# Performance work log

Hardware: AMD Instinct MI355X
Metric: run time of the kernel (lower is better)

Reference implementation:

```python
import jax, jax.numpy as jnp
import numpy as np

D_MODEL = 768
N_HEAD = 12
D_K = D_MODEL // N_HEAD  # 64, also d_v
B, S = 2, 2048


def setup_inputs() -> dict:
    key = jax.random.key(0)
    ks = jax.random.split(key, 8)
    scale = 1.0 / np.sqrt(D_MODEL)
    return {
        "q": jax.random.normal(ks[0], (B, S, D_MODEL), dtype=jnp.float32),
        "k": jax.random.normal(ks[1], (B, S, D_MODEL), dtype=jnp.float32),
        "v": jax.random.normal(ks[2], (B, S, D_MODEL), dtype=jnp.float32),
        "mask": jax.random.randint(ks[3], (B, 1, S, S), 0, 2, dtype=jnp.int32),
        # per-head projection weights, stacked over heads: [H, d_model, d_k]
        "Wq": jax.random.normal(ks[4], (N_HEAD, D_MODEL, D_K), dtype=jnp.float32) * scale,
        "Wk": jax.random.normal(ks[5], (N_HEAD, D_MODEL, D_K), dtype=jnp.float32) * scale,
        "Wv": jax.random.normal(ks[6], (N_HEAD, D_MODEL, D_K), dtype=jnp.float32) * scale,
        # output projection: [n_head*d_v, d_model]
        "Wo": jax.random.normal(ks[7], (N_HEAD * D_K, D_MODEL), dtype=jnp.float32) * scale,
    }


def reference(q, k, v, mask, Wq, Wk, Wv, Wo):
    # Per-head projections (batched over heads instead of a python loop)
    qh = jnp.einsum("bsd,hdk->bhsk", q, Wq)  # [B,H,S,d_k]
    kh = jnp.einsum("bsd,hdk->bhsk", k, Wk)
    vh = jnp.einsum("bsd,hdk->bhsk", v, Wv)
    # Scaled dot-product attention with full score matrix (faithful to source)
    scores = jnp.einsum("bhsk,bhtk->bhst", qh, kh) / jnp.sqrt(jnp.asarray(D_K, qh.dtype))
    scores = jnp.where(mask == 0, jnp.asarray(-1e9, scores.dtype), scores)
    attn = jax.nn.softmax(scores, axis=-1)  # [B,H,S,S]
    out = jnp.einsum("bhst,bhtk->bhsk", attn, vh)  # [B,H,S,d_k]
    # concat heads (matches torch.cat over head outputs along last dim)
    out = out.transpose(0, 2, 1, 3).reshape(out.shape[0], out.shape[2], -1)  # [B,S,H*d_k]
    return out @ Wo  # [B,S,d_model]
```

## Files before the change

### kernel.cpp

```cpp
#include <hip/hip_runtime.h>
#include <stdint.h>

#define S_LEN 2048
#define NH 12
#define DM 768
#define DK 64
#define NB 2
#define MROWS (NB * S_LEN)

typedef __attribute__((ext_vector_type(8))) short short8;
typedef __attribute__((ext_vector_type(4))) float f32x4;
typedef __attribute__((ext_vector_type(4))) uint32_t u32x4;

__device__ __forceinline__ unsigned short bf16rne(float f) {
    union { float f; uint32_t u; } v; v.f = f;
    return (unsigned short)((v.u + 0x7FFFu + ((v.u >> 16) & 1u)) >> 16);
}

__device__ __forceinline__ uint32_t cvtpk(float lo, float hi) {
    uint32_t r;
    asm("v_cvt_pk_bf16_f32 %0, %1, %2" : "=v"(r) : "v"(lo), "v"(hi));
    return r;
}

__global__ __launch_bounds__(256) void prep_kernel(
        const float* __restrict__ Wq, const float* __restrict__ Wk,
        const float* __restrict__ Wv, const float* __restrict__ Wo,
        const int* __restrict__ mask,
        unsigned short* __restrict__ WqT, unsigned short* __restrict__ WkT,
        unsigned short* __restrict__ WvT, unsigned short* __restrict__ WoT,
        uint32_t* __restrict__ pm) {
    const int bx = blockIdx.x, tid = threadIdx.x;
    if (bx < 576) {
        __shared__ __align__(16) unsigned short L[64 * 72];
        int kd0, n0;
        unsigned short* WT;
        if (bx < 432) {
            int which = bx / 144;
            int t2 = bx % 144;
            int h = t2 / 12; kd0 = (t2 % 12) * 64; n0 = h * 64;
            const float* W = (which == 0) ? Wq : (which == 1) ? Wk : Wv;
            WT = (which == 0) ? WqT : (which == 1) ? WkT : WvT;
            const int r = tid >> 2, c0 = (tid & 3) << 4;
            const size_t roff = ((size_t)(h * 768 + kd0 + r)) * 64 + c0;
            float4 f[4];
#pragma unroll
            for (int i = 0; i < 4; ++i) f[i] = *(const float4*)(W + roff + i * 4);
            const float scl = (which == 0) ? 0.18033688011112042f : 1.0f;
#pragma unroll
            for (int i = 0; i < 4; ++i) {
                L[(c0 + i * 4 + 0) * 72 + r] = bf16rne(f[i].x * scl);
                L[(c0 + i * 4 + 1) * 72 + r] = bf16rne(f[i].y * scl);
                L[(c0 + i * 4 + 2) * 72 + r] = bf16rne(f[i].z * scl);
                L[(c0 + i * 4 + 3) * 72 + r] = bf16rne(f[i].w * scl);
            }
        } else {
            int t3 = bx - 432;
            kd0 = (t3 / 12) * 64; n0 = (t3 % 12) * 64;
            WT = WoT;
            const int r = tid >> 2, c0 = (tid & 3) << 4;
            const size_t roff = ((size_t)(kd0 + r)) * 768 + n0 + c0;
            float4 f[4];
#pragma unroll
            for (int i = 0; i < 4; ++i) f[i] = *(const float4*)(Wo + roff + i * 4);
#pragma unroll
            for (int i = 0; i < 4; ++i) {
                L[(c0 + i * 4 + 0) * 72 + r] = bf16rne(f[i].x);
                L[(c0 + i * 4 + 1) * 72 + r] = bf16rne(f[i].y);
                L[(c0 + i * 4 + 2) * 72 + r] = bf16rne(f[i].z);
                L[(c0 + i * 4 + 3) * 72 + r] = bf16rne(f[i].w);
            }
        }
        __syncthreads();
        const int nl = tid >> 2, cc = (tid & 3) << 4;
        short8 v0 = *(const short8*)&L[nl * 72 + cc];
        short8 v1 = *(const short8*)&L[nl * 72 + cc + 8];
        *(short8*)&WT[(size_t)(n0 + nl) * DM + kd0 + cc] = v0;
        *(short8*)&WT[(size_t)(n0 + nl) * DM + kd0 + cc + 8] = v1;
    } else {
        int t = (bx - 576) * 256 + tid;
        const int4* mp = (const int4*)mask;
        int4 a = mp[2 * t], b = mp[2 * t + 1];
        unsigned int by =
            (a.x != 0 ? 1u : 0u)  | (a.y != 0 ? 2u : 0u)  | (a.z != 0 ? 4u : 0u)  | (a.w != 0 ? 8u : 0u) |
            (b.x != 0 ? 16u : 0u) | (b.y != 0 ? 32u : 0u) | (b.z != 0 ? 64u : 0u) | (b.w != 0 ? 128u : 0u);
        ((unsigned char*)pm)[t] = (unsigned char)by;
    }
}

__global__ __launch_bounds__(256) void proj_gemm(
        const float* __restrict__ qf32, const float* __restrict__ kf32,
        const float* __restrict__ vf32,
        const unsigned short* __restrict__ WqT, const unsigned short* __restrict__ WkT,
        const unsigned short* __restrict__ WvT,
        unsigned short* __restrict__ qh, unsigned short* __restrict__ kh,
        unsigned short* __restrict__ vhT) {
    __shared__ __align__(16) unsigned short As[2][128 * 32];
    __shared__ __align__(16) unsigned short Bs[2][64 * 32];
    const int bid = blockIdx.x;
    const int xcd = bid & 7, pos = bid >> 3;
    const int widx = xcd * 144 + pos;
    const int oi = widx / 12, by = widx % 12;
    const int z = oi >> 5, bx = oi & 31;
    const float* A = (z == 0) ? qf32 : (z == 1) ? kf32 : vf32;
    const unsigned short* BT = (z == 0) ? WqT : (z == 1) ? WkT : WvT;
    const int tid = threadIdx.x;
    const int lane = tid & 63, wid = tid >> 6;
    const int ww = wid & 1, wh = wid >> 1;
    const int quad = lane >> 4, l16 = lane & 15;
    const int lr = lane >> 2, lc = (lane & 3) * 8;
    typedef __attribute__((address_space(1))) const unsigned int* gp1;
    typedef __attribute__((address_space(3))) unsigned int* lp3;
    const int ar = tid >> 1, ahk = (tid & 1) * 16;
    const float* Ag = A + (size_t)(bx * 128 + ar) * DM + ahk;
    const int aoff = ar * 32 + ahk;
    const unsigned short* Bg = BT + (size_t)(by * 64 + wid * 16 + lr) * DM + lc;
    const int boff = wid * 16 * 32;

    f32x4 acc[4][2] = {};
    {
        float4 x0 = *(const float4*)(Ag);     float4 x1 = *(const float4*)(Ag + 4);
        float4 x2 = *(const float4*)(Ag + 8); float4 x3 = *(const float4*)(Ag + 12);
        __builtin_amdgcn_global_load_lds((gp1)(const void*)Bg, (lp3)(void*)&Bs[0][boff], 16, 0, 0);
        u32x4 u0, u1;
        u0[0] = cvtpk(x0.x, x0.y); u0[1] = cvtpk(x0.z, x0.w);
        u0[2] = cvtpk(x1.x, x1.y); u0[3] = cvtpk(x1.z, x1.w);
        u1[0] = cvtpk(x2.x, x2.y); u1[1] = cvtpk(x2.z, x2.w);
        u1[2] = cvtpk(x3.x, x3.y); u1[3] = cvtpk(x3.z, x3.w);
        *(u32x4*)&As[0][aoff] = u0;
        *(u32x4*)&As[0][aoff + 8] = u1;
    }
    __syncthreads();
    int cur = 0;
    for (int kt = 0; kt < DM; kt += 32) {
        const bool more = (kt + 32) < DM;
        float4 x0, x1, x2, x3;
        if (more) {
            x0 = *(const float4*)(Ag + kt + 32); x1 = *(const float4*)(Ag + kt + 36);
            x2 = *(const float4*)(Ag + kt + 40); x3 = *(const float4*)(Ag + kt + 44);
            __builtin_amdgcn_global_load_lds((gp1)(const void*)(Bg + kt + 32), (lp3)(void*)&Bs[cur ^ 1][boff], 16, 0, 0);
        }
        short8 af[4], bf[2];
#pragma unroll
        for (int i = 0; i < 4; ++i) af[i] = *(const short8*)&As[cur][(wh * 64 + i * 16 + l16) * 32 + quad * 8];
#pragma unroll
        for (int j = 0; j < 2; ++j) bf[j] = *(const short8*)&Bs[cur][(ww * 32 + j * 16 + l16) * 32 + quad * 8];
#pragma unroll
        for (int i = 0; i < 4; ++i)
#pragma unroll
            for (int j = 0; j < 2; ++j)
                acc[i][j] = __builtin_amdgcn_mfma_f32_16x16x32_bf16(af[i], bf[j], acc[i][j], 0, 0, 0);
        if (more) {
            u32x4 u0, u1;
            u0[0] = cvtpk(x0.x, x0.y); u0[1] = cvtpk(x0.z, x0.w);
            u0[2] = cvtpk(x1.x, x1.y); u0[3] = cvtpk(x1.z, x1.w);
            u1[0] = cvtpk(x2.x, x2.y); u1[1] = cvtpk(x2.z, x2.w);
            u1[2] = cvtpk(x3.x, x3.y); u1[3] = cvtpk(x3.z, x3.w);
            *(u32x4*)&As[cur ^ 1][aoff] = u0;
            *(u32x4*)&As[cur ^ 1][aoff + 8] = u1;
            __syncthreads();
            cur ^= 1;
        }
    }

    const int row0 = bx * 128 + wh * 64;
    const int col0 = by * 64 + ww * 32;
    if (z < 2) {
        unsigned short* C = z ? kh : qh;
#pragma unroll
        for (int i = 0; i < 4; ++i)
#pragma unroll
            for (int j = 0; j < 2; ++j)
#pragma unroll
                for (int r = 0; r < 4; ++r)
                    C[(size_t)(row0 + i * 16 + quad * 4 + r) * DM + col0 + j * 16 + l16] = bf16rne(acc[i][j][r]);
    } else {
#pragma unroll
        for (int i = 0; i < 4; ++i)
#pragma unroll
            for (int j = 0; j < 2; ++j) {
                int row = row0 + i * 16 + quad * 4;
                int col = col0 + j * 16 + l16;
                int bb = row >> 11, s = row & 2047;
                int hh = col >> 6, d = col & 63;
                int g = (s >> 2) & 15;
                int pg = (g & 8) | ((g & 3) << 1) | ((g & 4) >> 2);
                int sp = (s & ~63) | (pg << 2) | (s & 3);
                uint32_t lo = (uint32_t)bf16rne(acc[i][j][0]) | ((uint32_t)bf16rne(acc[i][j][1]) << 16);
                uint32_t hi = (uint32_t)bf16rne(acc[i][j][2]) | ((uint32_t)bf16rne(acc[i][j][3]) << 16);
                uint2 o = make_uint2(lo, hi);
                *(uint2*)&vhT[(size_t)((bb * NH + hh) * DK + d) * S_LEN + sp] = o;
            }
    }
}

__global__ __launch_bounds__(256) void attn_kernel(
        const unsigned short* __restrict__ qh, const unsigned short* __restrict__ kh,
        const unsigned short* __restrict__ vhT, const uint32_t* __restrict__ pm,
        unsigned short* __restrict__ pob, float* __restrict__ lsb) {
    const int bid = blockIdx.x;
    const int xcd = bid & 7, pos = bid >> 3;
    const int wkr = xcd * 192 + pos;
    const int qt = wkr & 15;
    const int hz = wkr >> 4;
    const int h = hz % 12;
    const int z = hz / 12;
    const int b = z >> 2, ks = z & 3;
    const int tid = threadIdx.x, w = tid >> 6, lane = tid & 63;
    const int quad = lane >> 4, l16 = lane & 15;
    __shared__ __align__(16) unsigned short SMEM[2 * 2 * 64 * 64];

    const int qrow0 = qt * 128 + w * 32;
    short8 qf[2][2];
#pragma unroll
    for (int mi = 0; mi < 2; ++mi) {
        const size_t qbase = (size_t)(b * S_LEN + qrow0 + mi * 16 + l16) * DM + h * DK;
        qf[mi][0] = *(const short8*)&qh[qbase + quad * 8];
        qf[mi][1] = *(const short8*)&qh[qbase + 32 + quad * 8];
    }
    short8 of = {};
    if (l16 == 0) {
#pragma unroll
        for (int j = 0; j < 8; ++j) of[j] = (short)0x3F80;
    }

    f32x4 out_t[2][4] = {};
    f32x4 outl[2] = {};

    const int srow = tid >> 2, scol = (tid & 3) << 4;
    const int ssw = (srow & 7) << 3;
    const int sc0 = srow * 64 + (scol ^ ssw);
    const int sc1 = srow * 64 + ((scol + 8) ^ ssw);
    const unsigned short* Kg = kh + (size_t)b * S_LEN * DM + h * DK;
    const unsigned short* Vg = vhT + (size_t)((b * NH + h) * DK) * S_LEN;
    const int kt0 = ks * (S_LEN / 4);
    const int NT = (S_LEN / 4) / 64;

    {
        short8 a0 = *(const short8*)&Kg[(size_t)(kt0 + srow) * DM + scol];
        short8 a1 = *(const short8*)&Kg[(size_t)(kt0 + srow) * DM + scol + 8];
        short8 a2 = *(const short8*)&Vg[(size_t)srow * S_LEN + kt0 + scol];
        short8 a3 = *(const short8*)&Vg[(size_t)srow * S_LEN + kt0 + scol + 8];
        *(short8*)&SMEM[sc0] = a0;
        *(short8*)&SMEM[sc1] = a1;
        *(short8*)&SMEM[4096 + sc0] = a2;
        *(short8*)&SMEM[4096 + sc1] = a3;
    }
    __syncthreads();

    int cur = 0;
    for (int t = 0; t < NT; ++t) {
        const int kt = kt0 + t * 64;
        const bool more = (t + 1 < NT);
        short8 kr0, kr1, vr0, vr1;
        if (more) {
            const int kn = kt + 64;
            kr0 = *(const short8*)&Kg[(size_t)(kn + srow) * DM + scol];
            kr1 = *(const short8*)&Kg[(size_t)(kn + srow) * DM + scol + 8];
            vr0 = *(const short8*)&Vg[(size_t)srow * S_LEN + kn + scol];
            vr1 = *(const short8*)&Vg[(size_t)srow * S_LEN + kn + scol + 8];
        }
        uint2 mw[2];
#pragma unroll
        for (int mi = 0; mi < 2; ++mi)
            mw[mi] = *(const uint2*)&pm[(size_t)(b * S_LEN + qrow0 + mi * 16 + l16) * 64 + (kt >> 5)];

        const unsigned short* Ks = SMEM + cur * 8192;
        const unsigned short* Vs = Ks + 4096;

        u32x4 pf32[2][2];
#pragma unroll
        for (int cb = 0; cb < 4; ++cb) {
            const int krw = cb * 16 + l16, ksw = (krw & 7) << 3;
            short8 kf0 = *(const short8*)&Ks[krw * 64 + ((quad * 8) ^ ksw)];
            short8 kf1 = *(const short8*)&Ks[krw * 64 + ((32 + quad * 8) ^ ksw)];
#pragma unroll
            for (int mi = 0; mi < 2; ++mi) {
                f32x4 zz = {0.f, 0.f, 0.f, 0.f};
                zz = __builtin_amdgcn_mfma_f32_16x16x32_bf16(kf0, qf[mi][0], zz, 0, 0, 0);
                zz = __builtin_amdgcn_mfma_f32_16x16x32_bf16(kf1, qf[mi][1], zz, 0, 0, 0);
                uint32_t mword = (cb & 2) ? mw[mi].y : mw[mi].x;
                float e[4];
#pragma unroll
                for (int r = 0; r < 4; ++r) {
                    float ev = __builtin_amdgcn_exp2f(zz[r]);
                    int32_t mneg = __builtin_amdgcn_sbfe((int32_t)mword, ((cb & 1) << 4) + quad * 4 + r, 1);
                    e[r] = __uint_as_float(__float_as_uint(ev) & (uint32_t)mneg);
                }
                pf32[mi][cb >> 1][(cb & 1) * 2 + 0] = cvtpk(e[0], e[1]);
                pf32[mi][cb >> 1][(cb & 1) * 2 + 1] = cvtpk(e[2], e[3]);
            }
        }
        short8 pf[2][2];
#pragma unroll
        for (int mi = 0; mi < 2; ++mi) {
            pf[mi][0] = __builtin_bit_cast(short8, pf32[mi][0]);
            pf[mi][1] = __builtin_bit_cast(short8, pf32[mi][1]);
        }

        __builtin_amdgcn_s_setprio(1);
#pragma unroll
        for (int c2 = 0; c2 < 4; ++c2) {
            const int vrw = c2 * 16 + l16, vsw = (vrw & 7) << 3;
            short8 vf0 = *(const short8*)&Vs[vrw * 64 + ((quad * 8) ^ vsw)];
            short8 vf1 = *(const short8*)&Vs[vrw * 64 + ((32 + quad * 8) ^ vsw)];
#pragma unroll
            for (int mi = 0; mi < 2; ++mi) {
                out_t[mi][c2] = __builtin_amdgcn_mfma_f32_16x16x32_bf16(vf0, pf[mi][0], out_t[mi][c2], 0, 0, 0);
                out_t[mi][c2] = __builtin_amdgcn_mfma_f32_16x16x32_bf16(vf1, pf[mi][1], out_t[mi][c2], 0, 0, 0);
            }
        }
#pragma unroll
        for (int mi = 0; mi < 2; ++mi) {
            outl[mi] = __builtin_amdgcn_mfma_f32_16x16x32_bf16(of, pf[mi][0], outl[mi], 0, 0, 0);
            outl[mi] = __builtin_amdgcn_mfma_f32_16x16x32_bf16(of, pf[mi][1], outl[mi], 0, 0, 0);
        }
        __builtin_amdgcn_s_setprio(0);

        if (more) {
            unsigned short* Kn = SMEM + (cur ^ 1) * 8192;
            *(short8*)&Kn[sc0] = kr0;
            *(short8*)&Kn[sc1] = kr1;
            *(short8*)&Kn[4096 + sc0] = vr0;
            *(short8*)&Kn[4096 + sc1] = vr1;
            __syncthreads();
            cur ^= 1;
        }
    }

    const int pz = z;
    if (quad == 0) {
#pragma unroll
        for (int mi = 0; mi < 2; ++mi)
            lsb[((size_t)pz * NH + h) * S_LEN + qrow0 + mi * 16 + l16] = outl[mi][0];
    }

    __syncthreads();
    unsigned short* Os = SMEM + w * 2048;
#pragma unroll
    for (int mi = 0; mi < 2; ++mi) {
        const int orow = mi * 16 + l16, osw = (orow & 7) << 3;
#pragma unroll
        for (int c2 = 0; c2 < 4; ++c2) {
            uint2 pw2;
            pw2.x = cvtpk(out_t[mi][c2][0], out_t[mi][c2][1]);
            pw2.y = cvtpk(out_t[mi][c2][2], out_t[mi][c2][3]);
            *(uint2*)&Os[orow * 64 + ((c2 * 16 + quad * 4) ^ osw)] = pw2;
        }
    }
    const int ql = lane >> 1, hf = lane & 1;
    const int qsw = (ql & 7) << 3;
    const int qg = qrow0 + ql;
    const size_t orowg = ((size_t)pz * S_LEN + qg) * DM + h * DK + hf * 32;
#pragma unroll
    for (int k2 = 0; k2 < 4; ++k2)
        *(short8*)&pob[orowg + k2 * 8] = *(const short8*)&Os[ql * 64 + ((hf * 32 + k2 * 8) ^ qsw)];
}

__global__ __launch_bounds__(256) void merge_kernel(const unsigned short* __restrict__ pob,
                                                    const float* __restrict__ lsb,
                                                    unsigned short* __restrict__ ao) {
    int t = blockIdx.x * 256 + threadIdx.x;
    int sg = t / 192;
    int c = (t - sg * 192) * 4;
    int b = sg >> 11, s = sg & 2047, h = c >> 6;
    float l = 0.f;
#pragma unroll
    for (int ksp = 0; ksp < 4; ++ksp)
        l += lsb[((size_t)(b * 4 + ksp) * NH + h) * S_LEN + s];
    float rl = 1.f / fmaxf(l, 1e-37f);
    float f0 = 0.f, f1 = 0.f, f2 = 0.f, f3 = 0.f;
#pragma unroll
    for (int ksp = 0; ksp < 4; ++ksp) {
        uint2 a = *(const uint2*)&pob[((size_t)((b * 4 + ksp) * S_LEN) + s) * DM + c];
        f0 += __uint_as_float(a.x << 16);
        f1 += __uint_as_float(a.x & 0xFFFF0000u);
        f2 += __uint_as_float(a.y << 16);
        f3 += __uint_as_float(a.y & 0xFFFF0000u);
    }
    uint32_t lo = cvtpk(f0 * rl, f1 * rl);
    uint32_t hi = cvtpk(f2 * rl, f3 * rl);
    *(uint2*)&ao[(size_t)sg * DM + c] = make_uint2(lo, hi);
}

__global__ __launch_bounds__(256) void out_gemm(
        const unsigned short* __restrict__ ao, const unsigned short* __restrict__ WoT,
        float* __restrict__ C) {
    __shared__ __align__(16) unsigned short As[2][64 * 32];
    __shared__ __align__(16) unsigned short Bs[2][64 * 32];
    const int bid = blockIdx.x;
    const int xcd = bid & 7, pos = bid >> 3;
    const int widx = xcd * 96 + pos;
    const int bx = widx / 12, by = widx % 12;
    const int tid = threadIdx.x;
    const int lane = tid & 63, wid = tid >> 6;
    const int ww = wid & 1, wh = wid >> 1;
    const int quad = lane >> 4, l16 = lane & 15;
    const int lr = lane >> 2, lc = (lane & 3) * 8;
    typedef __attribute__((address_space(1))) const unsigned int* gp1;
    typedef __attribute__((address_space(3))) unsigned int* lp3;
    const unsigned short* Ag = ao  + (size_t)(bx * 64 + wid * 16 + lr) * DM + lc;
    const unsigned short* Bg = WoT + (size_t)(by * 64 + wid * 16 + lr) * DM + lc;
    const int soff = wid * 16 * 32;
    f32x4 acc[2][2] = {};
    __builtin_amdgcn_global_load_lds((gp1)(const void*)Ag, (lp3)(void*)&As[0][soff], 16, 0, 0);
    __builtin_amdgcn_global_load_lds((gp1)(const void*)Bg, (lp3)(void*)&Bs[0][soff], 16, 0, 0);
    __syncthreads();
    int cur = 0;
    for (int kt = 0; kt < DM; kt += 32) {
        const bool more = (kt + 32) < DM;
        if (more) {
            __builtin_amdgcn_global_load_lds((gp1)(const void*)(Ag + kt + 32), (lp3)(void*)&As[cur ^ 1][soff], 16, 0, 0);
            __builtin_amdgcn_global_load_lds((gp1)(const void*)(Bg + kt + 32), (lp3)(void*)&Bs[cur ^ 1][soff], 16, 0, 0);
        }
        short8 af[2], bf[2];
#pragma unroll
        for (int i = 0; i < 2; ++i) af[i] = *(const short8*)&As[cur][(wh * 32 + i * 16 + l16) * 32 + quad * 8];
#pragma unroll
        for (int j = 0; j < 2; ++j) bf[j] = *(const short8*)&Bs[cur][(ww * 32 + j * 16 + l16) * 32 + quad * 8];
#pragma unroll
        for (int i = 0; i < 2; ++i)
#pragma unroll
            for (int j = 0; j < 2; ++j)
                acc[i][j] = __builtin_amdgcn_mfma_f32_16x16x32_bf16(af[i], bf[j], acc[i][j], 0, 0, 0);
        if (more) {
            __syncthreads();
            cur ^= 1;
        }
    }
    const int row0 = bx * 64 + wh * 32;
    const int col0 = by * 64 + ww * 32;
#pragma unroll
    for (int i = 0; i < 2; ++i)
#pragma unroll
        for (int j = 0; j < 2; ++j)
#pragma unroll
            for (int r = 0; r < 4; ++r)
                C[(size_t)(row0 + i * 16 + quad * 4 + r) * DM + col0 + j * 16 + l16] = acc[i][j][r];
}

extern "C" void kernel_launch(void* const* d_in, const int* in_sizes, int n_in,
                              void* d_out, int out_size, void* d_ws, size_t ws_size,
                              hipStream_t stream) {
    const float* q = (const float*)d_in[0];
    const float* k = (const float*)d_in[1];
    const float* v = (const float*)d_in[2];
    const int* mask = (const int*)d_in[3];
    const float* Wq = (const float*)d_in[4];
    const float* Wk = (const float*)d_in[5];
    const float* Wv = (const float*)d_in[6];
    const float* Wo = (const float*)d_in[7];
    float* out = (float*)d_out;

    char* ws = (char*)d_ws;
    size_t off = 0;
    auto alloc = [&](size_t bytes) {
        void* p = ws + off;
        off += (bytes + 255) & ~(size_t)255;
        return p;
    };
    const size_t MAT = (size_t)MROWS * DM * 2;
    const size_t WMAT = (size_t)DM * DM * 2;
    unsigned short* WoT = (unsigned short*)alloc(WMAT);
    unsigned short* qh  = (unsigned short*)alloc(MAT);
    unsigned short* kh  = (unsigned short*)alloc(MAT);
    unsigned short* vhT = (unsigned short*)alloc(MAT);
    uint32_t* pmask     = (uint32_t*)alloc((size_t)NB * S_LEN * 64 * 4);
    float* lsb          = (float*)alloc((size_t)8 * NH * S_LEN * 4);
    unsigned short* WqT = (unsigned short*)alloc(WMAT);
    unsigned short* WkT = (unsigned short*)alloc(WMAT);
    unsigned short* WvT = (unsigned short*)alloc(WMAT);
    unsigned short* pob = WqT;
    (void)alloc((size_t)8 * S_LEN * DM * 2 - 3 * WMAT);
    unsigned short* ao = qh;

    prep_kernel<<<dim3(576 + 4096), 256, 0, stream>>>(Wq, Wk, Wv, Wo, mask,
                                                      WqT, WkT, WvT, WoT, pmask);
    proj_gemm<<<dim3(1152), 256, 0, stream>>>(q, k, v, WqT, WkT, WvT, qh, kh, vhT);
    attn_kernel<<<dim3(1536), 256, 0, stream>>>(qh, kh, vhT, pmask, pob, lsb);
    merge_kernel<<<dim3(3072), 256, 0, stream>>>(pob, lsb, ao);
    out_gemm<<<dim3(768), 256, 0, stream>>>(ao, WoT, out);
}
```

Measured before the change: 232.9 us.

## Load GEMM operands directly from global into MFMA fragments, dropping LDS staging

Result: slower. 362.2 us (+55.5%).

```diff
diff --git a/kernel.cpp b/kernel.cpp
--- a/kernel.cpp
+++ b/kernel.cpp
@@ -95,8 +95,6 @@
         const unsigned short* __restrict__ WvT,
         unsigned short* __restrict__ qh, unsigned short* __restrict__ kh,
         unsigned short* __restrict__ vhT) {
-    __shared__ __align__(16) unsigned short As[2][128 * 32];
-    __shared__ __align__(16) unsigned short Bs[2][64 * 32];
     const int bid = blockIdx.x;
     const int xcd = bid & 7, pos = bid >> 3;
     const int widx = xcd * 144 + pos;
@@ -108,59 +106,36 @@
     const int lane = tid & 63, wid = tid >> 6;
     const int ww = wid & 1, wh = wid >> 1;
     const int quad = lane >> 4, l16 = lane & 15;
-    const int lr = lane >> 2, lc = (lane & 3) * 8;
-    typedef __attribute__((address_space(1))) const unsigned int* gp1;
-    typedef __attribute__((address_space(3))) unsigned int* lp3;
-    const int ar = tid >> 1, ahk = (tid & 1) * 16;
-    const float* Ag = A + (size_t)(bx * 128 + ar) * DM + ahk;
-    const int aoff = ar * 32 + ahk;
-    const unsigned short* Bg = BT + (size_t)(by * 64 + wid * 16 + lr) * DM + lc;
-    const int boff = wid * 16 * 32;
+
+    const float* Ab[4];
+#pragma unroll
+    for (int i = 0; i < 4; ++i)
+        Ab[i] = A + (size_t)(bx * 128 + wh * 64 + i * 16 + l16) * DM + quad * 8;
+    const unsigned short* Bb[2];
+#pragma unroll
+    for (int j = 0; j < 2; ++j)
+        Bb[j] = BT + (size_t)(by * 64 + ww * 32 + j * 16 + l16) * DM + quad * 8;
 
     f32x4 acc[4][2] = {};
-    {
-        float4 x0 = *(const float4*)(Ag);     float4 x1 = *(const float4*)(Ag + 4);
-        float4 x2 = *(const float4*)(Ag + 8); float4 x3 = *(const float4*)(Ag + 12);
-        __builtin_amdgcn_global_load_lds((gp1)(const void*)Bg, (lp3)(void*)&Bs[0][boff], 16, 0, 0);
-        u32x4 u0, u1;
-        u0[0] = cvtpk(x0.x, x0.y); u0[1] = cvtpk(x0.z, x0.w);
-        u0[2] = cvtpk(x1.x, x1.y); u0[3] = cvtpk(x1.z, x1.w);
-        u1[0] = cvtpk(x2.x, x2.y); u1[1] = cvtpk(x2.z, x2.w);
-        u1[2] = cvtpk(x3.x, x3.y); u1[3] = cvtpk(x3.z, x3.w);
-        *(u32x4*)&As[0][aoff] = u0;
-        *(u32x4*)&As[0][aoff + 8] = u1;
-    }
-    __syncthreads();
-    int cur = 0;
+#pragma unroll 4
     for (int kt = 0; kt < DM; kt += 32) {
-        const bool more = (kt + 32) < DM;
-        float4 x0, x1, x2, x3;
-        if (more) {
-            x0 = *(const float4*)(Ag + kt + 32); x1 = *(const float4*)(Ag + kt + 36);
-            x2 = *(const float4*)(Ag + kt + 40); x3 = *(const float4*)(Ag + kt + 44);
-            __builtin_amdgcn_global_load_lds((gp1)(const void*)(Bg + kt + 32), (lp3)(void*)&Bs[cur ^ 1][boff], 16, 0, 0);
-        }
         short8 af[4], bf[2];
 #pragma unroll
-        for (int i = 0; i < 4; ++i) af[i] = *(const short8*)&As[cur][(wh * 64 + i * 16 + l16) * 32 + quad * 8];
-#pragma unroll
-        for (int j = 0; j < 2; ++j) bf[j] = *(const short8*)&Bs[cur][(ww * 32 + j * 16 + l16) * 32 + quad * 8];
+        for (int i = 0; i < 4; ++i) {
+            float4 lo = *(const float4*)(Ab[i] + kt);
+            float4 hi = *(const float4*)(Ab[i] + kt + 4);
+            u32x4 u;
+            u[0] = cvtpk(lo.x, lo.y); u[1] = cvtpk(lo.z, lo.w);
+            u[2] = cvtpk(hi.x, hi.y); u[3] = cvtpk(hi.z, hi.w);
+            af[i] = __builtin_bit_cast(short8, u);
+        }
+#pragma unroll
+        for (int j = 0; j < 2; ++j) bf[j] = *(const short8*)(Bb[j] + kt);
 #pragma unroll
         for (int i = 0; i < 4; ++i)
 #pragma unroll
             for (int j = 0; j < 2; ++j)
                 acc[i][j] = __builtin_amdgcn_mfma_f32_16x16x32_bf16(af[i], bf[j], acc[i][j], 0, 0, 0);
-        if (more) {
-            u32x4 u0, u1;
-            u0[0] = cvtpk(x0.x, x0.y); u0[1] = cvtpk(x0.z, x0.w);
-            u0[2] = cvtpk(x1.x, x1.y); u0[3] = cvtpk(x1.z, x1.w);
-            u1[0] = cvtpk(x2.x, x2.y); u1[1] = cvtpk(x2.z, x2.w);
-            u1[2] = cvtpk(x3.x, x3.y); u1[3] = cvtpk(x3.z, x3.w);
-            *(u32x4*)&As[cur ^ 1][aoff] = u0;
-            *(u32x4*)&As[cur ^ 1][aoff + 8] = u1;
-            __syncthreads();
-            cur ^= 1;
-        }
     }
 
     const int row0 = bx * 128 + wh * 64;
@@ -386,8 +361,6 @@
 __global__ __launch_bounds__(256) void out_gemm(
         const unsigned short* __restrict__ ao, const unsigned short* __restrict__ WoT,
         float* __restrict__ C) {
-    __shared__ __align__(16) unsigned short As[2][64 * 32];
-    __shared__ __align__(16) unsigned short Bs[2][64 * 32];
     const int bid = blockIdx.x;
     const int xcd = bid & 7, pos = bid >> 3;
     const int widx = xcd * 96 + pos;
@@ -396,37 +369,27 @@
     const int lane = tid & 63, wid = tid >> 6;
     const int ww = wid & 1, wh = wid >> 1;
     const int quad = lane >> 4, l16 = lane & 15;
-    const int lr = lane >> 2, lc = (lane & 3) * 8;
-    typedef __attribute__((address_space(1))) const unsigned int* gp1;
-    typedef __attribute__((address_space(3))) unsigned int* lp3;
-    const unsigned short* Ag = ao  + (size_t)(bx * 64 + wid * 16 + lr) * DM + lc;
-    const unsigned short* Bg = WoT + (size_t)(by * 64 + wid * 16 + lr) * DM + lc;
-    const int soff = wid * 16 * 32;
+    const unsigned short* Ab[2];
+    const unsigned short* Bb[2];
+#pragma unroll
+    for (int i = 0; i < 2; ++i)
+        Ab[i] = ao + (size_t)(bx * 64 + wh * 32 + i * 16 + l16) * DM + quad * 8;
+#pragma unroll
+    for (int j = 0; j < 2; ++j)
+        Bb[j] = WoT + (size_t)(by * 64 + ww * 32 + j * 16 + l16) * DM + quad * 8;
     f32x4 acc[2][2] = {};
-    __builtin_amdgcn_global_load_lds((gp1)(const void*)Ag, (lp3)(void*)&As[0][soff], 16, 0, 0);
-    __builtin_amdgcn_global_load_lds((gp1)(const void*)Bg, (lp3)(void*)&Bs[0][soff], 16, 0, 0);
-    __syncthreads();
-    int cur = 0;
+#pragma unroll 8
     for (int kt = 0; kt < DM; kt += 32) {
-        const bool more = (kt + 32) < DM;
-        if (more) {
-            __builtin_amdgcn_global_load_lds((gp1)(const void*)(Ag + kt + 32), (lp3)(void*)&As[cur ^ 1][soff], 16, 0, 0);
-            __builtin_amdgcn_global_load_lds((gp1)(const void*)(Bg + kt + 32), (lp3)(void*)&Bs[cur ^ 1][soff], 16, 0, 0);
-        }
         short8 af[2], bf[2];
 #pragma unroll
-        for (int i = 0; i < 2; ++i) af[i] = *(const short8*)&As[cur][(wh * 32 + i * 16 + l16) * 32 + quad * 8];
-#pragma unroll
-        for (int j = 0; j < 2; ++j) bf[j] = *(const short8*)&Bs[cur][(ww * 32 + j * 16 + l16) * 32 + quad * 8];
+        for (int i = 0; i < 2; ++i) af[i] = *(const short8*)(Ab[i] + kt);
+#pragma unroll
+        for (int j = 0; j < 2; ++j) bf[j] = *(const short8*)(Bb[j] + kt);
 #pragma unroll
         for (int i = 0; i < 2; ++i)
 #pragma unroll
             for (int j = 0; j < 2; ++j)
                 acc[i][j] = __builtin_amdgcn_mfma_f32_16x16x32_bf16(af[i], bf[j], acc[i][j], 0, 0, 0);
-        if (more) {
-            __syncthreads();
-            cur ^= 1;
-        }
     }
     const int row0 = bx * 64 + wh * 32;
     const int col0 = by * 64 + ww * 32;
```

## Widen projection GEMM tile to 128x128 and drop LDS double buffering

Applied to the files above, without the earlier changes.

Result: faster. 214.5 us (-7.9%).

```diff
diff --git a/kernel.cpp b/kernel.cpp
--- a/kernel.cpp
+++ b/kernel.cpp
@@ -88,6 +88,50 @@
     }
 }
 
+__device__ __forceinline__ void gemm_core_f32A(const float* __restrict__ A,
+                                               const unsigned short* __restrict__ BT,
+                                               unsigned short* As, unsigned short* Bs,
+                                               f32x4 (&acc)[4][4]) {
+    const int tid = threadIdx.x;
+    const int lane = tid & 63, wid = tid >> 6;
+    const int ww = wid & 1, wh = wid >> 1;
+    const int quad = lane >> 4, l16 = lane & 15;
+    const int lr = lane >> 2;
+    const int lc = (lane & 3) * 8;
+    typedef __attribute__((address_space(1))) const unsigned int* gp1;
+    typedef __attribute__((address_space(3))) unsigned int* lp3;
+    const float* Ag0 = A + (size_t)(wid * 32 + lr) * DM + lc;
+    const float* Ag1 = A + (size_t)(wid * 32 + 16 + lr) * DM + lc;
+    const unsigned short* Bg = BT + (size_t)(wid * 32 + lr) * DM + lc;
+    unsigned short* Al = &As[wid * 32 * 32];
+    unsigned short* Bl = &Bs[wid * 32 * 32];
+    for (int kt = 0; kt < DM; kt += 32) {
+        __syncthreads();
+        __builtin_amdgcn_global_load_lds((gp1)(const void*)(Bg + kt),            (lp3)(void*)Bl,             16, 0, 0);
+        __builtin_amdgcn_global_load_lds((gp1)(const void*)(Bg + 16 * DM + kt),  (lp3)(void*)(Bl + 16 * 32), 16, 0, 0);
+        float4 x0 = *(const float4*)(Ag0 + kt), x1 = *(const float4*)(Ag0 + kt + 4);
+        float4 y0 = *(const float4*)(Ag1 + kt), y1 = *(const float4*)(Ag1 + kt + 4);
+        u32x4 ua, ub;
+        ua[0] = cvtpk(x0.x, x0.y); ua[1] = cvtpk(x0.z, x0.w);
+        ua[2] = cvtpk(x1.x, x1.y); ua[3] = cvtpk(x1.z, x1.w);
+        ub[0] = cvtpk(y0.x, y0.y); ub[1] = cvtpk(y0.z, y0.w);
+        ub[2] = cvtpk(y1.x, y1.y); ub[3] = cvtpk(y1.z, y1.w);
+        *(u32x4*)&Al[lr * 32 + lc] = ua;
+        *(u32x4*)&Al[(16 + lr) * 32 + lc] = ub;
+        __syncthreads();
+        short8 af[4], bf[4];
+#pragma unroll
+        for (int i = 0; i < 4; ++i) af[i] = *(const short8*)&As[(wh * 64 + i * 16 + l16) * 32 + quad * 8];
+#pragma unroll
+        for (int j = 0; j < 4; ++j) bf[j] = *(const short8*)&Bs[(ww * 64 + j * 16 + l16) * 32 + quad * 8];
+#pragma unroll
+        for (int i = 0; i < 4; ++i)
+#pragma unroll
+            for (int j = 0; j < 4; ++j)
+                acc[i][j] = __builtin_amdgcn_mfma_f32_16x16x32_bf16(af[i], bf[j], acc[i][j], 0, 0, 0);
+    }
+}
+
 __global__ __launch_bounds__(256) void proj_gemm(
         const float* __restrict__ qf32, const float* __restrict__ kf32,
         const float* __restrict__ vf32,
@@ -95,82 +139,30 @@
         const unsigned short* __restrict__ WvT,
         unsigned short* __restrict__ qh, unsigned short* __restrict__ kh,
         unsigned short* __restrict__ vhT) {
-    __shared__ __align__(16) unsigned short As[2][128 * 32];
-    __shared__ __align__(16) unsigned short Bs[2][64 * 32];
+    __shared__ __align__(16) unsigned short As[128 * 32];
+    __shared__ __align__(16) unsigned short Bs[128 * 32];
     const int bid = blockIdx.x;
     const int xcd = bid & 7, pos = bid >> 3;
-    const int widx = xcd * 144 + pos;
-    const int oi = widx / 12, by = widx % 12;
+    const int widx = xcd * 72 + pos;
+    const int oi = widx / 6, by = widx % 6;
     const int z = oi >> 5, bx = oi & 31;
     const float* A = (z == 0) ? qf32 : (z == 1) ? kf32 : vf32;
     const unsigned short* BT = (z == 0) ? WqT : (z == 1) ? WkT : WvT;
+    f32x4 acc[4][4] = {};
+    gemm_core_f32A(A + (size_t)bx * 128 * DM, BT + (size_t)by * 128 * DM, As, Bs, acc);
+
     const int tid = threadIdx.x;
     const int lane = tid & 63, wid = tid >> 6;
     const int ww = wid & 1, wh = wid >> 1;
     const int quad = lane >> 4, l16 = lane & 15;
-    const int lr = lane >> 2, lc = (lane & 3) * 8;
-    typedef __attribute__((address_space(1))) const unsigned int* gp1;
-    typedef __attribute__((address_space(3))) unsigned int* lp3;
-    const int ar = tid >> 1, ahk = (tid & 1) * 16;
-    const float* Ag = A + (size_t)(bx * 128 + ar) * DM + ahk;
-    const int aoff = ar * 32 + ahk;
-    const unsigned short* Bg = BT + (size_t)(by * 64 + wid * 16 + lr) * DM + lc;
-    const int boff = wid * 16 * 32;
-
-    f32x4 acc[4][2] = {};
-    {
-        float4 x0 = *(const float4*)(Ag);     float4 x1 = *(const float4*)(Ag + 4);
-        float4 x2 = *(const float4*)(Ag + 8); float4 x3 = *(const float4*)(Ag + 12);
-        __builtin_amdgcn_global_load_lds((gp1)(const void*)Bg, (lp3)(void*)&Bs[0][boff], 16, 0, 0);
-        u32x4 u0, u1;
-        u0[0] = cvtpk(x0.x, x0.y); u0[1] = cvtpk(x0.z, x0.w);
-        u0[2] = cvtpk(x1.x, x1.y); u0[3] = cvtpk(x1.z, x1.w);
-        u1[0] = cvtpk(x2.x, x2.y); u1[1] = cvtpk(x2.z, x2.w);
-        u1[2] = cvtpk(x3.x, x3.y); u1[3] = cvtpk(x3.z, x3.w);
-        *(u32x4*)&As[0][aoff] = u0;
-        *(u32x4*)&As[0][aoff + 8] = u1;
-    }
-    __syncthreads();
-    int cur = 0;
-    for (int kt = 0; kt < DM; kt += 32) {
-        const bool more = (kt + 32) < DM;
-        float4 x0, x1, x2, x3;
-        if (more) {
-            x0 = *(const float4*)(Ag + kt + 32); x1 = *(const float4*)(Ag + kt + 36);
-            x2 = *(const float4*)(Ag + kt + 40); x3 = *(const float4*)(Ag + kt + 44);
-            __builtin_amdgcn_global_load_lds((gp1)(const void*)(Bg + kt + 32), (lp3)(void*)&Bs[cur ^ 1][boff], 16, 0, 0);
-        }
-        short8 af[4], bf[2];
-#pragma unroll
-        for (int i = 0; i < 4; ++i) af[i] = *(const short8*)&As[cur][(wh * 64 + i * 16 + l16) * 32 + quad * 8];
-#pragma unroll
-        for (int j = 0; j < 2; ++j) bf[j] = *(const short8*)&Bs[cur][(ww * 32 + j * 16 + l16) * 32 + quad * 8];
-#pragma unroll
-        for (int i = 0; i < 4; ++i)
-#pragma unroll
-            for (int j = 0; j < 2; ++j)
-                acc[i][j] = __builtin_amdgcn_mfma_f32_16x16x32_bf16(af[i], bf[j], acc[i][j], 0, 0, 0);
-        if (more) {
-            u32x4 u0, u1;
-            u0[0] = cvtpk(x0.x, x0.y); u0[1] = cvtpk(x0.z, x0.w);
-            u0[2] = cvtpk(x1.x, x1.y); u0[3] = cvtpk(x1.z, x1.w);
-            u1[0] = cvtpk(x2.x, x2.y); u1[1] = cvtpk(x2.z, x2.w);
-            u1[2] = cvtpk(x3.x, x3.y); u1[3] = cvtpk(x3.z, x3.w);
-            *(u32x4*)&As[cur ^ 1][aoff] = u0;
-            *(u32x4*)&As[cur ^ 1][aoff + 8] = u1;
-            __syncthreads();
-            cur ^= 1;
-        }
-    }
-
     const int row0 = bx * 128 + wh * 64;
-    const int col0 = by * 64 + ww * 32;
+    const int col0 = by * 128 + ww * 64;
     if (z < 2) {
         unsigned short* C = z ? kh : qh;
 #pragma unroll
         for (int i = 0; i < 4; ++i)
 #pragma unroll
-            for (int j = 0; j < 2; ++j)
+            for (int j = 0; j < 4; ++j)
 #pragma unroll
                 for (int r = 0; r < 4; ++r)
                     C[(size_t)(row0 + i * 16 + quad * 4 + r) * DM + col0 + j * 16 + l16] = bf16rne(acc[i][j][r]);
@@ -178,7 +170,7 @@
 #pragma unroll
         for (int i = 0; i < 4; ++i)
 #pragma unroll
-            for (int j = 0; j < 2; ++j) {
+            for (int j = 0; j < 4; ++j) {
                 int row = row0 + i * 16 + quad * 4;
                 int col = col0 + j * 16 + l16;
                 int bb = row >> 11, s = row & 2047;
@@ -476,7 +468,7 @@
 
     prep_kernel<<<dim3(576 + 4096), 256, 0, stream>>>(Wq, Wk, Wv, Wo, mask,
                                                       WqT, WkT, WvT, WoT, pmask);
-    proj_gemm<<<dim3(1152), 256, 0, stream>>>(q, k, v, WqT, WkT, WvT, qh, kh, vhT);
+    proj_gemm<<<dim3(576), 256, 0, stream>>>(q, k, v, WqT, WkT, WvT, qh, kh, vhT);
     attn_kernel<<<dim3(1536), 256, 0, stream>>>(qh, kh, vhT, pmask, pob, lsb);
     merge_kernel<<<dim3(3072), 256, 0, stream>>>(pob, lsb, ao);
     out_gemm<<<dim3(768), 256, 0, stream>>>(ao, WoT, out);
```
